# Kernel tuning notes

Measured on AMD Instinct MI355X. Metric: run time of the kernel, lower is better.

The kernel has to match this reference:

```python
import jax, jax.numpy as jnp
import numpy as np

N_HEADS = 32
KV_HEADS = 8
HEAD_DIM = 128
N_REP = N_HEADS // KV_HEADS


def _rope(x, cos, sin):
    # x: [b, s, h, d]; cos/sin: [s, d//2]
    xr = x[..., 0::2]
    xi = x[..., 1::2]
    c = cos[None, :, None, :]
    s = sin[None, :, None, :]
    or_ = xr * c - xi * s
    oi_ = xr * s + xi * c
    return jnp.stack([or_, oi_], axis=-1).reshape(x.shape)


def setup_inputs() -> dict:
    key = jax.random.key(0)
    ks = jax.random.split(key, 9)
    b, s, dim = 32, 1, 4096
    scale = 1.0 / np.sqrt(dim)
    inp = {
        "x": jax.random.normal(ks[0], (b, s, dim), jnp.float32),
        "wq": jax.random.normal(ks[1], (4096, 4096), jnp.float32) * scale,
        "wk": jax.random.normal(ks[2], (1024, 4096), jnp.float32) * scale,
        "wv": jax.random.normal(ks[3], (1024, 4096), jnp.float32) * scale,
        "wo": jax.random.normal(ks[4], (4096, 4096), jnp.float32) * scale,
        "freqs_cos": jax.random.uniform(ks[5], (s, HEAD_DIM // 2), jnp.float32),
        "freqs_sin": jax.random.uniform(ks[6], (s, HEAD_DIM // 2), jnp.float32),
        "cache_k": jax.random.normal(ks[7], (32, 2048, KV_HEADS, HEAD_DIM), jnp.float32),
        "cache_v": jax.random.normal(ks[8], (32, 2048, KV_HEADS, HEAD_DIM), jnp.float32),
        "start_pos": 2047,
    }
    return inp


def reference(x, wq, wk, wv, wo, freqs_cos, freqs_sin, cache_k, cache_v, start_pos):
    b, s, dim = x.shape
    # projections (nn.Linear: y = x @ W^T)
    xq = (x @ wq.T).reshape(b, s, N_HEADS, HEAD_DIM)
    xk = (x @ wk.T).reshape(b, s, KV_HEADS, HEAD_DIM)
    xv = (x @ wv.T).reshape(b, s, KV_HEADS, HEAD_DIM)
    # inline RoPE on q and k
    xq = _rope(xq, freqs_cos, freqs_sin)
    xk = _rope(xk, freqs_cos, freqs_sin)
    # KV-cache write (start_pos is a static Python int)
    cache_k = cache_k.at[:b, start_pos:start_pos + s].set(xk)
    cache_v = cache_v.at[:b, start_pos:start_pos + s].set(xv)
    t = start_pos + s
    keys = cache_k[:b, :t]    # [b, t, kv, d]
    values = cache_v[:b, :t]  # [b, t, kv, d]
    # GQA: group queries per kv head instead of materializing repeat_kv copies
    q = xq.reshape(b, s, KV_HEADS, N_REP, HEAD_DIM)
    scores = jnp.einsum("bqhrd,bkhd->bhrqk", q, keys) / np.sqrt(HEAD_DIM)
    probs = jax.nn.softmax(scores.astype(jnp.float32), axis=-1).astype(xq.dtype)
    out = jnp.einsum("bhrqk,bkhd->bqhrd", probs, values)
    out = out.reshape(b, s, N_HEADS * HEAD_DIM)
    return out @ wo.T
```

## Files before the change

kernel.cpp:

```cpp
#include <hip/hip_runtime.h>
#include <hip/hip_bf16.h>
#include <math.h>

#define KSPLIT 16
#define KCHUNK 256
#define BJ 128
#define TSPLIT 4

__global__ __launch_bounds__(256) void gemv_part_kernel(
    const float* __restrict__ x,
    const float* __restrict__ w0,
    const float* __restrict__ w1,
    const float* __restrict__ w2,
    int jb1, int jb2,
    int off0, int off1, int off2,
    int ncols,
    float* __restrict__ part)
{
  __shared__ float xt[KCHUNK][32];
  int jb = blockIdx.x, ks = blockIdx.y;
  int k0 = ks * KCHUNK;
  const float* w; int colOff, jbase;
  if (jb < jb1)      { w = w0; colOff = off0; jbase = jb * BJ; }
  else if (jb < jb2) { w = w1; colOff = off1; jbase = (jb - jb1) * BJ; }
  else               { w = w2; colOff = off2; jbase = (jb - jb2) * BJ; }
  int tid = threadIdx.x;
  {
    int b = tid & 31, kg = tid >> 5;
    const float* xr = x + (size_t)b * 4096 + k0 + kg * 32;
    #pragma unroll
    for (int i = 0; i < 8; i++) {
      float4 v = *(const float4*)(xr + i * 4);
      int k = kg * 32 + i * 4;
      xt[k + 0][b] = v.x; xt[k + 1][b] = v.y;
      xt[k + 2][b] = v.z; xt[k + 3][b] = v.w;
    }
  }
  __syncthreads();
  int bg = tid & 7, jg = tid >> 3;
  const float* wb = w + (size_t)(jbase + jg * 4) * 4096 + k0;
  float acc[4][4] = {};
  #pragma unroll 4
  for (int k4 = 0; k4 < KCHUNK / 4; k4++) {
    float wr[4][4], xv[4][4];
    #pragma unroll
    for (int jj = 0; jj < 4; jj++) {
      float4 t = *(const float4*)(wb + (size_t)jj * 4096 + k4 * 4);
      wr[jj][0] = t.x; wr[jj][1] = t.y; wr[jj][2] = t.z; wr[jj][3] = t.w;
    }
    #pragma unroll
    for (int c = 0; c < 4; c++) {
      float4 t = *(const float4*)(&xt[k4 * 4 + c][bg * 4]);
      xv[c][0] = t.x; xv[c][1] = t.y; xv[c][2] = t.z; xv[c][3] = t.w;
    }
    #pragma unroll
    for (int jj = 0; jj < 4; jj++)
      #pragma unroll
      for (int bb = 0; bb < 4; bb++)
        acc[jj][bb] += wr[jj][0] * xv[0][bb] + wr[jj][1] * xv[1][bb]
                     + wr[jj][2] * xv[2][bb] + wr[jj][3] * xv[3][bb];
  }
  #pragma unroll
  for (int jj = 0; jj < 4; jj++) {
    int col = colOff + jbase + jg * 4 + jj;
    #pragma unroll
    for (int bb = 0; bb < 4; bb++) {
      int b_ = bg * 4 + bb;
      part[((size_t)ks * 32 + b_) * ncols + col] = acc[jj][bb];
    }
  }
}

__global__ __launch_bounds__(256) void reduce_rope_kernel(
    const float* __restrict__ part, int ncols,
    const float* __restrict__ cosv, const float* __restrict__ sinv,
    int ropeEnd, float* __restrict__ outb)
{
  int idx = blockIdx.x * 256 + threadIdx.x;
  int np = ncols >> 1;
  int b = idx / np;
  int cp = idx - b * np;
  int col = cp * 2;
  float e = 0.f, o = 0.f;
  #pragma unroll
  for (int ks = 0; ks < KSPLIT; ks++) {
    float2 v = *(const float2*)(part + ((size_t)ks * 32 + b) * ncols + col);
    e += v.x; o += v.y;
  }
  if (col < ropeEnd) {
    int fi = (col & 127) >> 1;
    float c = cosv[fi], s = sinv[fi];
    float ne = e * c - o * s;
    float no = e * s + o * c;
    e = ne; o = no;
  }
  *(float2*)(outb + (size_t)b * ncols + col) = make_float2(e, o);
}

__global__ __launch_bounds__(256, 4) void attn_kernel(
    const float* __restrict__ qkv,
    const float* __restrict__ cache_k,
    const float* __restrict__ cache_v,
    const int* __restrict__ spp,
    float* __restrict__ attn_part)
{
  __shared__ float ktile[4][1024];
  __shared__ float q_sw[640];
  __shared__ float sbuf[4][64][4];
  __shared__ float kn_s[128], vn_s[128];

  int bid = blockIdx.x;
  int ts = bid & (TSPLIT - 1), h = (bid >> 2) & 7, b = bid >> 5;
  int sp = *spp;
  const float scale = 0.088388347648318447f;
  int tid = threadIdx.x;

  if (tid < 128) {
    int dq16 = tid & 31, r = tid >> 5;
    float4 qv = *(const float4*)(qkv + (size_t)b * 6144 + (h * 4 + r) * 128 + dq16 * 4);
    qv.x *= scale; qv.y *= scale; qv.z *= scale; qv.w *= scale;
    *(float4*)(&q_sw[dq16 * 20 + r * 4]) = qv;
  } else {
    int t2 = tid - 128;
    kn_s[t2] = qkv[(size_t)b * 6144 + 4096 + h * 128 + t2];
    vn_s[t2] = qkv[(size_t)b * 6144 + 5120 + h * 128 + t2];
  }
  __syncthreads();

  int wave = tid >> 6, lane = tid & 63;
  int half = lane >> 5, dq = lane & 31;
  int rl = lane >> 3, dg = lane & 7;
  float* kt = &ktile[wave][0];
  int base0 = ts * 512 + wave * 128;
  const float* Kb = cache_k + (size_t)b * 2048 * 1024 + h * 128;
  const float* Vb = cache_v + (size_t)b * 2048 * 1024 + h * 128;

  float m[4]    = {-INFINITY, -INFINITY, -INFINITY, -INFINITY};
  float lsum[4] = {0.f, 0.f, 0.f, 0.f};
  float o[4][4] = {};

  const int wr_byte = (dq * 16);
  char* ktc = (char*)kt;

  for (int c = 0; c < 2; c++) {
    int tbase = base0 + c * 64;
    const float* src0 = Kb + (size_t)(tbase + half) * 1024 + dq * 4;

    auto LOADK = [&](float4* dst, int st) {
      #pragma unroll
      for (int j = 0; j < 4; j++)
        dst[j] = *(const float4*)(src0 + (size_t)(st * 8 + j * 2) * 1024);
    };
    auto WRITEK = [&](const float4* srcv) {
      #pragma unroll
      for (int j = 0; j < 4; j++) {
        int rw = j * 2 + half;
        *(float4*)(ktc + rw * 512 + (wr_byte ^ (rw << 4))) = srcv[j];
      }
    };
    auto COMPUTEK = [&](int st) {
      float sp4[4] = {0.f, 0.f, 0.f, 0.f};
      #pragma unroll
      for (int i = 0; i < 4; i++) {
        float4 kv = *(const float4*)(ktc + rl * 512 + ((dg * 64 + i * 16) ^ (rl << 4)));
        int qo = (dg * 4 + i) * 20;
        #pragma unroll
        for (int r = 0; r < 4; r++) {
          float4 qv = *(const float4*)(&q_sw[qo + r * 4]);
          sp4[r] += kv.x * qv.x + kv.y * qv.y + kv.z * qv.z + kv.w * qv.w;
        }
      }
      #pragma unroll
      for (int r = 0; r < 4; r++) {
        sp4[r] += __shfl_xor(sp4[r], 1);
        sp4[r] += __shfl_xor(sp4[r], 2);
        sp4[r] += __shfl_xor(sp4[r], 4);
      }
      if (dg == 0)
        *(float4*)(&sbuf[wave][st * 8 + rl][0]) =
            make_float4(sp4[0], sp4[1], sp4[2], sp4[3]);
    };

    float4 st_reg[2][4];
    LOADK(st_reg[0], 0);
    LOADK(st_reg[1], 1);
    #pragma unroll
    for (int st = 0; st < 8; st++) {
      WRITEK(st_reg[st & 1]);
      if (st + 2 < 8) LOADK(st_reg[st & 1], st + 2);
      COMPUTEK(st);
    }

    int t = tbase + lane;
    float4 sv = *(const float4*)(&sbuf[wave][lane][0]);
    float s4[4] = {sv.x, sv.y, sv.z, sv.w};
    if (t >= sp) { s4[0] = s4[1] = s4[2] = s4[3] = -INFINITY; }
    float pv[4];
    #pragma unroll
    for (int r = 0; r < 4; r++) {
      float cm = s4[r];
      #pragma unroll
      for (int off = 32; off >= 1; off >>= 1) cm = fmaxf(cm, __shfl_xor(cm, off));
      float nm = fmaxf(m[r], cm);
      float alpha, p;
      if (nm == -INFINITY) { alpha = 1.f; p = 0.f; }
      else {
        alpha = __expf(m[r] - nm);
        p = (s4[r] == -INFINITY) ? 0.f : __expf(s4[r] - nm);
      }
      m[r] = nm;
      lsum[r] = lsum[r] * alpha + p;
      #pragma unroll
      for (int j = 0; j < 4; j++) o[r][j] *= alpha;
      pv[r] = p;
    }
    *(float4*)(&sbuf[wave][lane][0]) = make_float4(pv[0], pv[1], pv[2], pv[3]);

    #pragma unroll 8
    for (int tt = 0; tt < 32; tt++) {
      int tcur = tbase + tt * 2 + half;
      float4 vv = *(const float4*)(Vb + (size_t)tcur * 1024 + dq * 4);
      const float* pp = &sbuf[wave][tt * 2 + half][0];
      #pragma unroll
      for (int r = 0; r < 4; r++) {
        float p = pp[r];
        o[r][0] += p * vv.x; o[r][1] += p * vv.y;
        o[r][2] += p * vv.z; o[r][3] += p * vv.w;
      }
    }
  }

  if (wave == 0 && sp >= ts * 512 && sp < ts * 512 + 512) {
    float sNew[4];
    #pragma unroll
    for (int r = 0; r < 4; r++) {
      float4 qv4 = *(const float4*)(&q_sw[(lane >> 1) * 20 + r * 4]);
      float q0 = (lane & 1) ? qv4.z : qv4.x;
      float q1 = (lane & 1) ? qv4.w : qv4.y;
      float a = q0 * kn_s[lane * 2] + q1 * kn_s[lane * 2 + 1];
      #pragma unroll
      for (int off = 32; off >= 1; off >>= 1) a += __shfl_xor(a, off);
      sNew[r] = a;
    }
    #pragma unroll
    for (int r = 0; r < 4; r++) {
      float nm = fmaxf(m[r], sNew[r]);
      float alpha = (m[r] == -INFINITY) ? 0.f : __expf(m[r] - nm);
      float p = __expf(sNew[r] - nm);
      m[r] = nm;
      lsum[r] = lsum[r] * alpha + ((lane == 0) ? p : 0.f);
      float sel = (half == 0) ? p : 0.f;
      #pragma unroll
      for (int j = 0; j < 4; j++)
        o[r][j] = o[r][j] * alpha + sel * vn_s[dq * 4 + j];
    }
  }

  {
    float* comb = &ktile[wave][0];
    #pragma unroll
    for (int r = 0; r < 4; r++) {
      float L = lsum[r];
      #pragma unroll
      for (int off = 32; off >= 1; off >>= 1) L += __shfl_xor(L, off);
      #pragma unroll
      for (int j = 0; j < 4; j++) o[r][j] += __shfl_xor(o[r][j], 32);
      if (lane == 0) { comb[512 + r] = m[r]; comb[516 + r] = L; }
      if (half == 0) {
        #pragma unroll
        for (int j = 0; j < 4; j++) comb[r * 128 + dq * 4 + j] = o[r][j];
      }
    }
  }
  __syncthreads();
  {
    int r = tid >> 6, dp = tid & 63;
    float gm = fmaxf(fmaxf(ktile[0][512 + r], ktile[1][512 + r]),
                     fmaxf(ktile[2][512 + r], ktile[3][512 + r]));
    float L = 0.f, O0 = 0.f, O1 = 0.f;
    #pragma unroll
    for (int wv = 0; wv < 4; wv++) {
      float mm = ktile[wv][512 + r];
      float al = (mm == -INFINITY) ? 0.f : __expf(mm - gm);
      L  += ktile[wv][516 + r] * al;
      O0 += ktile[wv][r * 128 + dp * 2]     * al;
      O1 += ktile[wv][r * 128 + dp * 2 + 1] * al;
    }
    float* ap = attn_part + ((((size_t)ts * 32 + b) * 8 + h) * 4 + r) * 130;
    if (dp == 0) { ap[0] = gm; ap[1] = L; }
    ap[2 + dp * 2] = O0;
    ap[3 + dp * 2] = O1;
  }
}

__global__ __launch_bounds__(256) void attn_combine_kernel(
    const float* __restrict__ attn_part, float* __restrict__ attn)
{
  int idx = blockIdx.x * 256 + threadIdx.x;
  int d = idx & 127;
  int r = (idx >> 7) & 3;
  int h = (idx >> 9) & 7;
  int b = idx >> 12;
  float mv[TSPLIT], lv[TSPLIT], ov[TSPLIT];
  float gm = -INFINITY;
  #pragma unroll
  for (int ts = 0; ts < TSPLIT; ts++) {
    const float* ap = attn_part + (((size_t)(ts * 32 + b) * 8 + h) * 4 + r) * 130;
    mv[ts] = ap[0]; lv[ts] = ap[1]; ov[ts] = ap[2 + d];
    gm = fmaxf(gm, mv[ts]);
  }
  float L = 0.f, O = 0.f;
  #pragma unroll
  for (int ts = 0; ts < TSPLIT; ts++) {
    float al = (mv[ts] == -INFINITY) ? 0.f : __expf(mv[ts] - gm);
    L += lv[ts] * al;
    O += ov[ts] * al;
  }
  attn[idx] = O / L;
}

extern "C" void kernel_launch(void* const* d_in, const int* in_sizes, int n_in,
                              void* d_out, int out_size, void* d_ws, size_t ws_size,
                              hipStream_t stream)
{
  const float* x   = (const float*)d_in[0];
  const float* wq  = (const float*)d_in[1];
  const float* wk  = (const float*)d_in[2];
  const float* wv  = (const float*)d_in[3];
  const float* wo  = (const float*)d_in[4];
  const float* fc  = (const float*)d_in[5];
  const float* fs  = (const float*)d_in[6];
  const float* ck  = (const float*)d_in[7];
  const float* cv  = (const float*)d_in[8];
  const int*   spp = (const int*)d_in[9];
  float* out = (float*)d_out;

  float* ws = (float*)d_ws;
  float* qkv_part  = ws;
  float* out_part  = ws;
  float* qkvbuf    = ws + 3145728;
  float* attn_part = qkvbuf + 196608;
  float* attnbuf   = attn_part + 532480;

  gemv_part_kernel<<<dim3(48, KSPLIT), 256, 0, stream>>>(
      x, wq, wk, wv, 32, 40, 0, 4096, 5120, 6144, qkv_part);
  reduce_rope_kernel<<<384, 256, 0, stream>>>(qkv_part, 6144, fc, fs, 5120, qkvbuf);
  attn_kernel<<<1024, 256, 0, stream>>>(qkvbuf, ck, cv, spp, attn_part);
  attn_combine_kernel<<<512, 256, 0, stream>>>(attn_part, attnbuf);
  gemv_part_kernel<<<dim3(32, KSPLIT), 256, 0, stream>>>(
      attnbuf, wo, wo, wo, 32, 32, 0, 0, 0, 4096, out_part);
  reduce_rope_kernel<<<256, 256, 0, stream>>>(out_part, 4096, fc, fs, 0, out);
}
```

Before: 253.3 us.

## Keep Q in registers, read K directly from global, halve attention split

The attention kernel now holds the four query rows in registers and reads K straight from global memory into a triple-buffered register pipeline. This replaces the swizzled LDS K tile and the LDS query layout. V loads are also triple-buffered, and the score scaling moves to after the dot product. TSPLIT drops from 4 to 2, so each block covers 1024 timesteps and the grid is 512 blocks with launch bounds of 2 per SIMD. This gives fewer partials to combine and less LDS traffic, but it raises register pressure and halves the block-level parallelism available to hide memory latency.

```diff
diff --git a/kernel.cpp b/kernel.cpp
--- a/kernel.cpp
+++ b/kernel.cpp
@@ -5,7 +5,7 @@
 #define KSPLIT 16
 #define KCHUNK 256
 #define BJ 128
-#define TSPLIT 4
+#define TSPLIT 2
 
 __global__ __launch_bounds__(256) void gemv_part_kernel(
     const float* __restrict__ x,
@@ -97,150 +97,156 @@
   *(float2*)(outb + (size_t)b * ncols + col) = make_float2(e, o);
 }
 
-__global__ __launch_bounds__(256, 4) void attn_kernel(
+__global__ __launch_bounds__(256, 2) void attn_kernel(
     const float* __restrict__ qkv,
     const float* __restrict__ cache_k,
     const float* __restrict__ cache_v,
     const int* __restrict__ spp,
     float* __restrict__ attn_part)
 {
-  __shared__ float ktile[4][1024];
-  __shared__ float q_sw[640];
   __shared__ float sbuf[4][64][4];
   __shared__ float kn_s[128], vn_s[128];
+  __shared__ float comb[4][520];
 
   int bid = blockIdx.x;
-  int ts = bid & (TSPLIT - 1), h = (bid >> 2) & 7, b = bid >> 5;
+  int ts = bid & (TSPLIT - 1), h = (bid >> 1) & 7, b = bid >> 4;
   int sp = *spp;
   const float scale = 0.088388347648318447f;
   int tid = threadIdx.x;
 
-  if (tid < 128) {
-    int dq16 = tid & 31, r = tid >> 5;
-    float4 qv = *(const float4*)(qkv + (size_t)b * 6144 + (h * 4 + r) * 128 + dq16 * 4);
-    qv.x *= scale; qv.y *= scale; qv.z *= scale; qv.w *= scale;
-    *(float4*)(&q_sw[dq16 * 20 + r * 4]) = qv;
-  } else {
-    int t2 = tid - 128;
-    kn_s[t2] = qkv[(size_t)b * 6144 + 4096 + h * 128 + t2];
-    vn_s[t2] = qkv[(size_t)b * 6144 + 5120 + h * 128 + t2];
-  }
+  if (tid < 128)      kn_s[tid]       = qkv[(size_t)b * 6144 + 4096 + h * 128 + tid];
+  else                vn_s[tid - 128] = qkv[(size_t)b * 6144 + 5120 + h * 128 + tid - 128];
   __syncthreads();
 
   int wave = tid >> 6, lane = tid & 63;
   int half = lane >> 5, dq = lane & 31;
-  int rl = lane >> 3, dg = lane & 7;
-  float* kt = &ktile[wave][0];
-  int base0 = ts * 512 + wave * 128;
+  int tl = lane & 7,  dg = lane >> 3;
+  int base0 = ts * 1024 + wave * 256;
   const float* Kb = cache_k + (size_t)b * 2048 * 1024 + h * 128;
   const float* Vb = cache_v + (size_t)b * 2048 * 1024 + h * 128;
+
+  float4 qreg[4][4];
+  {
+    const float* qb = qkv + (size_t)b * 6144 + h * 512;
+    #pragma unroll
+    for (int r = 0; r < 4; r++)
+      #pragma unroll
+      for (int i = 0; i < 4; i++)
+        qreg[r][i] = *(const float4*)(qb + r * 128 + dg * 4 + i * 32);
+  }
 
   float m[4]    = {-INFINITY, -INFINITY, -INFINITY, -INFINITY};
   float lsum[4] = {0.f, 0.f, 0.f, 0.f};
   float o[4][4] = {};
 
-  const int wr_byte = (dq * 16);
-  char* ktc = (char*)kt;
-
-  for (int c = 0; c < 2; c++) {
+  for (int c = 0; c < 4; c++) {
     int tbase = base0 + c * 64;
-    const float* src0 = Kb + (size_t)(tbase + half) * 1024 + dq * 4;
-
-    auto LOADK = [&](float4* dst, int st) {
-      #pragma unroll
-      for (int j = 0; j < 4; j++)
-        dst[j] = *(const float4*)(src0 + (size_t)(st * 8 + j * 2) * 1024);
-    };
-    auto WRITEK = [&](const float4* srcv) {
-      #pragma unroll
-      for (int j = 0; j < 4; j++) {
-        int rw = j * 2 + half;
-        *(float4*)(ktc + rw * 512 + (wr_byte ^ (rw << 4))) = srcv[j];
+
+    {
+      const float* Krow = Kb + (size_t)(tbase + tl) * 1024 + dg * 4;
+      float4 kbuf[3][4];
+      auto LOADG = [&](int g, int buf) {
+        #pragma unroll
+        for (int i = 0; i < 4; i++)
+          kbuf[buf][i] = *(const float4*)(Krow + (size_t)g * 8192 + i * 32);
+      };
+      LOADG(0, 0); LOADG(1, 1);
+      #pragma unroll
+      for (int g = 0; g < 8; g++) {
+        if (g + 2 < 8) LOADG(g + 2, (g + 2) % 3);
+        const float4* kb = kbuf[g % 3];
+        float sp4[4] = {0.f, 0.f, 0.f, 0.f};
+        #pragma unroll
+        for (int i = 0; i < 4; i++)
+          #pragma unroll
+          for (int r = 0; r < 4; r++)
+            sp4[r] += kb[i].x * qreg[r][i].x + kb[i].y * qreg[r][i].y
+                    + kb[i].z * qreg[r][i].z + kb[i].w * qreg[r][i].w;
+        #pragma unroll
+        for (int r = 0; r < 4; r++) {
+          sp4[r] += __shfl_xor(sp4[r], 8);
+          sp4[r] += __shfl_xor(sp4[r], 16);
+          sp4[r] += __shfl_xor(sp4[r], 32);
+        }
+        if (dg == 0)
+          *(float4*)(&sbuf[wave][g * 8 + tl][0]) = make_float4(
+              sp4[0] * scale, sp4[1] * scale, sp4[2] * scale, sp4[3] * scale);
       }
-    };
-    auto COMPUTEK = [&](int st) {
-      float sp4[4] = {0.f, 0.f, 0.f, 0.f};
-      #pragma unroll
-      for (int i = 0; i < 4; i++) {
-        float4 kv = *(const float4*)(ktc + rl * 512 + ((dg * 64 + i * 16) ^ (rl << 4)));
-        int qo = (dg * 4 + i) * 20;
-        #pragma unroll
-        for (int r = 0; r < 4; r++) {
-          float4 qv = *(const float4*)(&q_sw[qo + r * 4]);
-          sp4[r] += kv.x * qv.x + kv.y * qv.y + kv.z * qv.z + kv.w * qv.w;
+    }
+
+    {
+      int t = tbase + lane;
+      float4 sv = *(const float4*)(&sbuf[wave][lane][0]);
+      float s4[4] = {sv.x, sv.y, sv.z, sv.w};
+      if (t >= sp) { s4[0] = s4[1] = s4[2] = s4[3] = -INFINITY; }
+      float pv[4];
+      #pragma unroll
+      for (int r = 0; r < 4; r++) {
+        float cm = s4[r];
+        #pragma unroll
+        for (int off = 32; off >= 1; off >>= 1) cm = fmaxf(cm, __shfl_xor(cm, off));
+        float nm = fmaxf(m[r], cm);
+        float alpha, p;
+        if (nm == -INFINITY) { alpha = 1.f; p = 0.f; }
+        else {
+          alpha = __expf(m[r] - nm);
+          p = (s4[r] == -INFINITY) ? 0.f : __expf(s4[r] - nm);
+        }
+        m[r] = nm;
+        lsum[r] = lsum[r] * alpha + p;
+        #pragma unroll
+        for (int j = 0; j < 4; j++) o[r][j] *= alpha;
+        pv[r] = p;
+      }
+      *(float4*)(&sbuf[wave][lane][0]) = make_float4(pv[0], pv[1], pv[2], pv[3]);
+    }
+
+    {
+      const float* Vsrc = Vb + (size_t)(tbase + half) * 1024 + dq * 4;
+      float4 vbuf[3][4];
+      auto LOADV = [&](int G, int buf) {
+        #pragma unroll
+        for (int j = 0; j < 4; j++)
+          vbuf[buf][j] = *(const float4*)(Vsrc + (size_t)(G * 8 + j * 2) * 1024);
+      };
+      LOADV(0, 0); LOADV(1, 1);
+      #pragma unroll
+      for (int G = 0; G < 8; G++) {
+        if (G + 2 < 8) LOADV(G + 2, (G + 2) % 3);
+        #pragma unroll
+        for (int j = 0; j < 4; j++) {
+          float4 vv = vbuf[G % 3][j];
+          float4 pp = *(const float4*)(&sbuf[wave][G * 8 + j * 2 + half][0]);
+          o[0][0] += pp.x * vv.x; o[0][1] += pp.x * vv.y;
+          o[0][2] += pp.x * vv.z; o[0][3] += pp.x * vv.w;
+          o[1][0] += pp.y * vv.x; o[1][1] += pp.y * vv.y;
+          o[1][2] += pp.y * vv.z; o[1][3] += pp.y * vv.w;
+          o[2][0] += pp.z * vv.x; o[2][1] += pp.z * vv.y;
+          o[2][2] += pp.z * vv.z; o[2][3] += pp.z * vv.w;
+          o[3][0] += pp.w * vv.x; o[3][1] += pp.w * vv.y;
+          o[3][2] += pp.w * vv.z; o[3][3] += pp.w * vv.w;
         }
       }
-      #pragma unroll
-      for (int r = 0; r < 4; r++) {
-        sp4[r] += __shfl_xor(sp4[r], 1);
-        sp4[r] += __shfl_xor(sp4[r], 2);
-        sp4[r] += __shfl_xor(sp4[r], 4);
-      }
-      if (dg == 0)
-        *(float4*)(&sbuf[wave][st * 8 + rl][0]) =
-            make_float4(sp4[0], sp4[1], sp4[2], sp4[3]);
-    };
-
-    float4 st_reg[2][4];
-    LOADK(st_reg[0], 0);
-    LOADK(st_reg[1], 1);
-    #pragma unroll
-    for (int st = 0; st < 8; st++) {
-      WRITEK(st_reg[st & 1]);
-      if (st + 2 < 8) LOADK(st_reg[st & 1], st + 2);
-      COMPUTEK(st);
-    }
-
-    int t = tbase + lane;
-    float4 sv = *(const float4*)(&sbuf[wave][lane][0]);
-    float s4[4] = {sv.x, sv.y, sv.z, sv.w};
-    if (t >= sp) { s4[0] = s4[1] = s4[2] = s4[3] = -INFINITY; }
-    float pv[4];
+    }
+  }
+
+  if (wave == 0 && sp >= ts * 1024 && sp < ts * 1024 + 1024) {
+    float4 kn4[4];
+    #pragma unroll
+    for (int i = 0; i < 4; i++)
+      kn4[i] = *(const float4*)(&kn_s[dg * 4 + i * 32]);
+    float sNew[4];
     #pragma unroll
     for (int r = 0; r < 4; r++) {
-      float cm = s4[r];
-      #pragma unroll
-      for (int off = 32; off >= 1; off >>= 1) cm = fmaxf(cm, __shfl_xor(cm, off));
-      float nm = fmaxf(m[r], cm);
-      float alpha, p;
-      if (nm == -INFINITY) { alpha = 1.f; p = 0.f; }
-      else {
-        alpha = __expf(m[r] - nm);
-        p = (s4[r] == -INFINITY) ? 0.f : __expf(s4[r] - nm);
-      }
-      m[r] = nm;
-      lsum[r] = lsum[r] * alpha + p;
-      #pragma unroll
-      for (int j = 0; j < 4; j++) o[r][j] *= alpha;
-      pv[r] = p;
-    }
-    *(float4*)(&sbuf[wave][lane][0]) = make_float4(pv[0], pv[1], pv[2], pv[3]);
-
-    #pragma unroll 8
-    for (int tt = 0; tt < 32; tt++) {
-      int tcur = tbase + tt * 2 + half;
-      float4 vv = *(const float4*)(Vb + (size_t)tcur * 1024 + dq * 4);
-      const float* pp = &sbuf[wave][tt * 2 + half][0];
-      #pragma unroll
-      for (int r = 0; r < 4; r++) {
-        float p = pp[r];
-        o[r][0] += p * vv.x; o[r][1] += p * vv.y;
-        o[r][2] += p * vv.z; o[r][3] += p * vv.w;
-      }
-    }
-  }
-
-  if (wave == 0 && sp >= ts * 512 && sp < ts * 512 + 512) {
-    float sNew[4];
-    #pragma unroll
-    for (int r = 0; r < 4; r++) {
-      float4 qv4 = *(const float4*)(&q_sw[(lane >> 1) * 20 + r * 4]);
-      float q0 = (lane & 1) ? qv4.z : qv4.x;
-      float q1 = (lane & 1) ? qv4.w : qv4.y;
-      float a = q0 * kn_s[lane * 2] + q1 * kn_s[lane * 2 + 1];
-      #pragma unroll
-      for (int off = 32; off >= 1; off >>= 1) a += __shfl_xor(a, off);
-      sNew[r] = a;
+      float a = 0.f;
+      #pragma unroll
+      for (int i = 0; i < 4; i++)
+        a += kn4[i].x * qreg[r][i].x + kn4[i].y * qreg[r][i].y
+           + kn4[i].z * qreg[r][i].z + kn4[i].w * qreg[r][i].w;
+      a += __shfl_xor(a, 8);
+      a += __shfl_xor(a, 16);
+      a += __shfl_xor(a, 32);
+      sNew[r] = a * scale;
     }
     #pragma unroll
     for (int r = 0; r < 4; r++) {
@@ -256,35 +262,32 @@
     }
   }
 
-  {
-    float* comb = &ktile[wave][0];
-    #pragma unroll
-    for (int r = 0; r < 4; r++) {
-      float L = lsum[r];
-      #pragma unroll
-      for (int off = 32; off >= 1; off >>= 1) L += __shfl_xor(L, off);
-      #pragma unroll
-      for (int j = 0; j < 4; j++) o[r][j] += __shfl_xor(o[r][j], 32);
-      if (lane == 0) { comb[512 + r] = m[r]; comb[516 + r] = L; }
-      if (half == 0) {
-        #pragma unroll
-        for (int j = 0; j < 4; j++) comb[r * 128 + dq * 4 + j] = o[r][j];
-      }
+  #pragma unroll
+  for (int r = 0; r < 4; r++) {
+    float L = lsum[r];
+    #pragma unroll
+    for (int off = 32; off >= 1; off >>= 1) L += __shfl_xor(L, off);
+    #pragma unroll
+    for (int j = 0; j < 4; j++) o[r][j] += __shfl_xor(o[r][j], 32);
+    if (lane == 0) { comb[wave][512 + r] = m[r]; comb[wave][516 + r] = L; }
+    if (half == 0) {
+      #pragma unroll
+      for (int j = 0; j < 4; j++) comb[wave][r * 128 + dq * 4 + j] = o[r][j];
     }
   }
   __syncthreads();
   {
     int r = tid >> 6, dp = tid & 63;
-    float gm = fmaxf(fmaxf(ktile[0][512 + r], ktile[1][512 + r]),
-                     fmaxf(ktile[2][512 + r], ktile[3][512 + r]));
+    float gm = fmaxf(fmaxf(comb[0][512 + r], comb[1][512 + r]),
+                     fmaxf(comb[2][512 + r], comb[3][512 + r]));
     float L = 0.f, O0 = 0.f, O1 = 0.f;
     #pragma unroll
     for (int wv = 0; wv < 4; wv++) {
-      float mm = ktile[wv][512 + r];
+      float mm = comb[wv][512 + r];
       float al = (mm == -INFINITY) ? 0.f : __expf(mm - gm);
-      L  += ktile[wv][516 + r] * al;
-      O0 += ktile[wv][r * 128 + dp * 2]     * al;
-      O1 += ktile[wv][r * 128 + dp * 2 + 1] * al;
+      L  += comb[wv][516 + r] * al;
+      O0 += comb[wv][r * 128 + dp * 2]     * al;
+      O1 += comb[wv][r * 128 + dp * 2 + 1] * al;
     }
     float* ap = attn_part + ((((size_t)ts * 32 + b) * 8 + h) * 4 + r) * 130;
     if (dp == 0) { ap[0] = gm; ap[1] = L; }
@@ -340,12 +343,12 @@
   float* out_part  = ws;
   float* qkvbuf    = ws + 3145728;
   float* attn_part = qkvbuf + 196608;
-  float* attnbuf   = attn_part + 532480;
+  float* attnbuf   = attn_part + 266240;
 
   gemv_part_kernel<<<dim3(48, KSPLIT), 256, 0, stream>>>(
       x, wq, wk, wv, 32, 40, 0, 4096, 5120, 6144, qkv_part);
   reduce_rope_kernel<<<384, 256, 0, stream>>>(qkv_part, 6144, fc, fs, 5120, qkvbuf);
-  attn_kernel<<<1024, 256, 0, stream>>>(qkvbuf, ck, cv, spp, attn_part);
+  attn_kernel<<<512, 256, 0, stream>>>(qkvbuf, ck, cv, spp, attn_part);
   attn_combine_kernel<<<512, 256, 0, stream>>>(attn_part, attnbuf);
   gemv_part_kernel<<<dim3(32, KSPLIT), 256, 0, stream>>>(
       attnbuf, wo, wo, wo, 32, 32, 0, 0, 0, 4096, out_part);
```

Result: faster. 220.2 us (-13.0%).
